# Kernel tuning notes

Hardware: AMD Instinct MI355X
Metric: run time of the kernel (lower is better)

The kernel has to match this reference:

```python
import jax, jax.numpy as jnp
import numpy as np
from jax import lax

B, L, D = 4, 4096, 1024
H = 4
DK = D // H   # head_k_dim = 256
DV = D // H   # head_v_dim = 256
HID = max(8, D // 2)  # gate trunk hidden = 512
CHUNK = 32
CONV_K = 4
EPS = 1e-5


def silu(x):
    return x * jax.nn.sigmoid(x)


def l2norm(x):
    return x * lax.rsqrt(jnp.sum(x * x, -1, keepdims=True) + 1e-6)


def causal_dwconv_silu(x, w):
    # x: (b,l,d), w: (d,k). Depthwise causal conv1d followed by SiLU (ShortConvolution).
    k = w.shape[-1]
    xp = jnp.pad(x, ((0, 0), (k - 1, 0), (0, 0))).transpose(0, 2, 1)  # (b,d,l+k-1)
    y = lax.conv_general_dilated(xp, w[:, None, :], (1,), 'VALID',
                                 feature_group_count=w.shape[0])
    return silu(y.transpose(0, 2, 1))


def delta_rule_chunkwise(q, k, v, beta, chunk=CHUNK):
    # q,k: (b,h,l,dk), v: (b,h,l,dv), beta: (b,h,l). l assumed multiple of chunk.
    b, h, l, dk = q.shape
    dv = v.shape[-1]
    n = l // chunk
    q = l2norm(q)
    k = l2norm(k)
    v = v * beta[..., None]
    kb = k * beta[..., None]
    qc = q.reshape(b, h, n, chunk, dk)
    kc = k.reshape(b, h, n, chunk, dk)
    vc = v.reshape(b, h, n, chunk, dv)
    kbc = kb.reshape(b, h, n, chunk, dk)
    # In-chunk triangular inverse: the torch loop computes (I + tril(kb k^T, -1))^{-1}
    Lm = jnp.tril(kbc @ jnp.swapaxes(kc, -1, -2), -1)  # strictly lower
    eye = jnp.eye(chunk, dtype=q.dtype)
    Tinv = jax.scipy.linalg.solve_triangular(eye + Lm, jnp.broadcast_to(eye, Lm.shape), lower=True)
    u = Tinv @ vc   # (b,h,n,c,dv)
    w = Tinv @ kbc  # (b,h,n,c,dk)
    strict = jnp.triu(jnp.ones((chunk, chunk), bool), 1)

    def step(S, inp):
        q_i, k_i, u_i, w_i = inp  # (b,h,c,d)
        attn = jnp.where(strict, 0.0, q_i @ jnp.swapaxes(k_i, -1, -2))
        u_hat = u_i - w_i @ S
        o_i = q_i @ S + attn @ u_hat
        return S + jnp.swapaxes(k_i, -1, -2) @ u_hat, o_i

    S0 = jnp.zeros((b, h, dk, dv), q.dtype)
    xs = tuple(jnp.moveaxis(t, 2, 0) for t in (qc, kc, u, w))
    S, o = lax.scan(step, S0, xs)
    o = jnp.moveaxis(o, 0, 2).reshape(b, h, l, dv)
    return o, S


def ema_rule(v, gamma):
    # v: (b,h,l,d), gamma: (b,h,l). Causal EMA: s_t = g_t*s_{t-1} + (1-g_t)*v_t
    def step(state, inp):
        v_t, g_t = inp
        state = g_t[..., None] * state + (1.0 - g_t[..., None]) * v_t
        return state, state

    s0 = jnp.zeros((v.shape[0], v.shape[1], v.shape[3]), v.dtype)
    _, out = lax.scan(step, s0, (jnp.moveaxis(v, 2, 0), jnp.moveaxis(gamma, 2, 0)))
    return jnp.moveaxis(out, 0, 2)


def hierarchical_gate(x, Wtrunk, btrunk, Wcoarse, bcoarse, Wlocal, blocal, Wglobal, bglobal, log_temp_c, log_temp_f):
    b, l, _ = x.shape
    z = silu(x @ Wtrunk.T + btrunk)  # (b,l,HID)
    tc = (jax.nn.softplus(log_temp_c) + 1e-4)[None, None, :, None]  # (1,1,h,1)
    tf = (jax.nn.softplus(log_temp_f) + 1e-4)[None, None, :, None]
    pg = jax.nn.softmax((z @ Wcoarse.T + bcoarse).reshape(b, l, H, 2) / tc, axis=-1)
    q = jax.nn.softmax((z @ Wlocal.T + blocal).reshape(b, l, H, 2) / tf, axis=-1)
    r = jax.nn.softmax((z @ Wglobal.T + bglobal).reshape(b, l, H, 2) / tf, axis=-1)
    w_v = pg[..., 0:1] * q[..., 0:1]
    w_es = pg[..., 0:1] * q[..., 1:2]
    w_d = pg[..., 1:2] * r[..., 0:1]
    w_el = pg[..., 1:2] * r[..., 1:2]
    return jnp.concatenate([w_v, w_es, w_d, w_el], axis=-1)  # (b,l,h,4)


def setup_inputs() -> dict:
    key = jax.random.key(0)
    ks = jax.random.split(key, 20)
    s = 0.02
    inp = {
        'hidden_states': jax.random.normal(ks[0], (B, L, D), jnp.float32),
        'Wq': jax.random.normal(ks[1], (D, D), jnp.float32) * s,
        'Wk': jax.random.normal(ks[2], (D, D), jnp.float32) * s,
        'Wv': jax.random.normal(ks[3], (D, D), jnp.float32) * s,
        'conv_q_w': jax.random.normal(ks[4], (D, CONV_K), jnp.float32) * 0.5,
        'conv_k_w': jax.random.normal(ks[5], (D, CONV_K), jnp.float32) * 0.5,
        'conv_v_w': jax.random.normal(ks[6], (D, CONV_K), jnp.float32) * 0.5,
        'Wb': jax.random.normal(ks[7], (H, D), jnp.float32) * s,
        'Wds': jax.random.normal(ks[8], (H, D), jnp.float32) * s,
        'bds': jnp.full((H,), -2.9444, jnp.float32),
        'Wdl': jax.random.normal(ks[9], (H, D), jnp.float32) * s,
        'bdl': jnp.full((H,), 2.9444, jnp.float32),
        'Wtrunk': jax.random.normal(ks[10], (HID, D), jnp.float32) * s,
        'btrunk': jnp.zeros((HID,), jnp.float32),
        'Wcoarse': jax.random.normal(ks[11], (H * 2, HID), jnp.float32) * s,
        'bcoarse': jnp.ones((H * 2,), jnp.float32),
        'Wlocal': jax.random.normal(ks[12], (H * 2, HID), jnp.float32) * s,
        'blocal': jnp.zeros((H * 2,), jnp.float32).at[::2].set(1.0),
        'Wglobal': jax.random.normal(ks[13], (H * 2, HID), jnp.float32) * s,
        'bglobal': jnp.zeros((H * 2,), jnp.float32).at[::2].set(1.0),
        'log_temp_c': jnp.zeros((H,), jnp.float32),  # log(1.0)
        'log_temp_f': jnp.zeros((H,), jnp.float32),
        'o_norm_w': jnp.ones((DV,), jnp.float32),
        'Wo': jax.random.normal(ks[14], (D, D), jnp.float32) * s,
    }
    return inp


def reference(hidden_states, Wq, Wk, Wv, conv_q_w, conv_k_w, conv_v_w, Wb, Wds, bds, Wdl, bdl,
              Wtrunk, btrunk, Wcoarse, bcoarse, Wlocal, blocal, Wglobal, bglobal,
              log_temp_c, log_temp_f, o_norm_w, Wo):
    x = hidden_states
    b, l, _ = x.shape
    # projections + short causal depthwise conv + SiLU
    q = causal_dwconv_silu(x @ Wq.T, conv_q_w).reshape(b, l, H, DK).transpose(0, 2, 1, 3)
    k = causal_dwconv_silu(x @ Wk.T, conv_k_w).reshape(b, l, H, DK).transpose(0, 2, 1, 3)
    v = causal_dwconv_silu(x @ Wv.T, conv_v_w).reshape(b, l, H, DV).transpose(0, 2, 1, 3)
    beta = jax.nn.sigmoid(x @ Wb.T).transpose(0, 2, 1)  # (b,h,l)
    delta_o, _ = delta_rule_chunkwise(q, k, v, beta)
    g_s = jax.nn.sigmoid(x @ Wds.T + bds).transpose(0, 2, 1)  # (b,h,l) short decay
    g_l = jax.nn.sigmoid(x @ Wdl.T + bdl).transpose(0, 2, 1)  # long decay
    ema_s = ema_rule(v, g_s)
    ema_l = ema_rule(v, g_l)
    weights = hierarchical_gate(x, Wtrunk, btrunk, Wcoarse, bcoarse, Wlocal, blocal,
                                Wglobal, bglobal, log_temp_c, log_temp_f)  # (b,l,h,4) [V,Es,D,El]
    v_b = v.transpose(0, 2, 1, 3)
    o = (weights[..., 0:1] * v_b
         + weights[..., 1:2] * ema_s.transpose(0, 2, 1, 3)
         + weights[..., 2:3] * delta_o.transpose(0, 2, 1, 3)
         + weights[..., 3:4] * ema_l.transpose(0, 2, 1, 3))
    # per-head RMSNorm
    o = o * lax.rsqrt(jnp.mean(o * o, -1, keepdims=True) + EPS) * o_norm_w
    return o.reshape(b, l, D) @ Wo.T
```

## Files before the change

kernel.cpp:

```cpp
#include <hip/hip_runtime.h>
#include <math.h>

#define BB 4
#define LL 4096
#define DD 1024
#define HH 4
#define DKk 256
#define DVv 256
#define HIDD 512
#define NC 128
#define NSEG 64
#define SEG 64

typedef unsigned short ushort_t;
typedef __attribute__((ext_vector_type(8))) short short8;
typedef __attribute__((ext_vector_type(4))) float floatx4;

__device__ __forceinline__ float sigm(float x) { return 1.f / (1.f + __expf(-x)); }

__device__ __forceinline__ float bf2f(ushort_t u) {
  union { unsigned int i; float f; } c; c.i = ((unsigned int)u) << 16; return c.f;
}
__device__ __forceinline__ ushort_t f2bf(float f) {
  union { float f; unsigned int i; } c; c.f = f;
  unsigned int lsb = (c.i >> 16) & 1u;
  return (ushort_t)((c.i + 0x7fffu + lsb) >> 16);
}
__device__ __forceinline__ void unpack2(unsigned int u, float& a, float& b) {
  union { unsigned int i; float f; } c0, c1;
  c0.i = u << 16; c1.i = u & 0xffff0000u; a = c0.f; b = c1.f;
}
__device__ __forceinline__ unsigned int pack2(float a, float b) {
  return (unsigned int)f2bf(a) | ((unsigned int)f2bf(b) << 16);
}
__device__ __forceinline__ void unpack8(const uint4 v, float* o) {
  unpack2(v.x, o[0], o[1]); unpack2(v.y, o[2], o[3]);
  unpack2(v.z, o[4], o[5]); unpack2(v.w, o[6], o[7]);
}
__device__ __forceinline__ float ubits(unsigned u) {
  union { unsigned i; float f; } c; c.i = u; return c.f;
}
__device__ __forceinline__ void split2t(float a, float b, unsigned& hi, unsigned& lo) {
  union { float f; unsigned u; } ca, cb; ca.f = a; cb.f = b;
  const unsigned ha = ca.u & 0xffff0000u, hb = cb.u & 0xffff0000u;
  hi = (ha >> 16) | hb;
  union { float f; unsigned u; } la, lb;
  la.f = a - ubits(ha); lb.f = b - ubits(hb);
  lo = (la.u >> 16) | (lb.u & 0xffff0000u);
}
__device__ __forceinline__ void gload16(const ushort_t* g, ushort_t* l) {
  __builtin_amdgcn_global_load_lds(
      (const __attribute__((address_space(1))) void*)g,
      (__attribute__((address_space(3))) void*)l, 16, 0, 0);
}

__global__ __launch_bounds__(256) void cvt_bf16_kernel(const float* __restrict__ in,
    ushort_t* __restrict__ outp, int n8)
{
  const int i = blockIdx.x * 256 + threadIdx.x;
  if (i >= n8) return;
  const float4 a = ((const float4*)in)[2*i];
  const float4 b = ((const float4*)in)[2*i + 1];
  uint4 p;
  p.x = pack2(a.x, a.y); p.y = pack2(a.z, a.w);
  p.z = pack2(b.x, b.y); p.w = pack2(b.z, b.w);
  ((uint4*)outp)[i] = p;
}

template<int ACT, int BF16OUT>
__global__ __launch_bounds__(256) void gemm_bf16(const ushort_t* __restrict__ A,
    const ushort_t* __restrict__ W, const float* __restrict__ bias,
    void* __restrict__ Cv, int M, int N, int K)
{
  __shared__ ushort_t As[128*32];
  __shared__ ushort_t Ws[128*32];
  const int tid = threadIdx.x;
  const int bm = blockIdx.y * 128, bn = blockIdx.x * 128;
  const int lane = tid & 63, wave = tid >> 6;
  const int wm = (wave >> 1) * 64, wn = (wave & 1) * 64;
  const int fr = lane & 15, fq = lane >> 4;
  const int srow = wave * 16 + (lane >> 2);
  const int scol = (lane & 3) * 8;
  const ushort_t* Ap = A + (size_t)(bm + srow) * K + scol;
  const ushort_t* Wp = W + (size_t)(bn + srow) * K + scol;
  ushort_t* AsD = &As[wave * 512];
  ushort_t* WsD = &Ws[wave * 512];
  floatx4 acc[4][4];
#pragma unroll
  for (int i = 0; i < 4; ++i)
#pragma unroll
    for (int j = 0; j < 4; ++j) acc[i][j] = (floatx4){0.f, 0.f, 0.f, 0.f};

  for (int k0 = 0; k0 < K; k0 += 32) {
    __syncthreads();
    gload16(Ap + k0, AsD);
    gload16(Ap + (size_t)64 * K + k0, AsD + 64*32);
    gload16(Wp + k0, WsD);
    gload16(Wp + (size_t)64 * K + k0, WsD + 64*32);
    __syncthreads();
    short8 af[4], bf_[4];
#pragma unroll
    for (int mt = 0; mt < 4; ++mt)
      af[mt] = *(const short8*)&As[(wm + mt*16 + fr)*32 + fq*8];
#pragma unroll
    for (int nt = 0; nt < 4; ++nt)
      bf_[nt] = *(const short8*)&Ws[(wn + nt*16 + fr)*32 + fq*8];
#pragma unroll
    for (int mt = 0; mt < 4; ++mt)
#pragma unroll
      for (int nt = 0; nt < 4; ++nt)
        acc[mt][nt] = __builtin_amdgcn_mfma_f32_16x16x32_bf16(af[mt], bf_[nt], acc[mt][nt], 0, 0, 0);
  }
#pragma unroll
  for (int mt = 0; mt < 4; ++mt) {
#pragma unroll
    for (int reg = 0; reg < 4; ++reg) {
      const int row = bm + wm + mt*16 + fq*4 + reg;
#pragma unroll
      for (int nt = 0; nt < 4; ++nt) {
        const int col = bn + wn + nt*16 + fr;
        float v = acc[mt][nt][reg];
        if (ACT == 1) { v += bias[col]; v = v * sigm(v); }
        if (BF16OUT) ((ushort_t*)Cv)[(size_t)row * N + col] = f2bf(v);
        else         ((float*)Cv)[(size_t)row * N + col] = v;
      }
    }
  }
}

__global__ __launch_bounds__(256) void conv_silu_kernel(const ushort_t* __restrict__ xin,
    const float* __restrict__ wc, ushort_t* __restrict__ outp)
{
  const size_t i8 = (size_t)blockIdx.x * 256 + threadIdx.x;
  const int d8 = (int)((i8 & 127) << 3);
  const int l  = (int)((i8 >> 7) & (LL - 1));
  const int b  = (int)(i8 >> 19);
  const ushort_t* xp = xin + i8 * 8;
  const uint4 z4 = (uint4){0u,0u,0u,0u};
  const uint4 v0 = *(const uint4*)xp;
  const uint4 v1 = (l >= 1) ? *(const uint4*)(xp - DD)   : z4;
  const uint4 v2 = (l >= 2) ? *(const uint4*)(xp - 2*DD) : z4;
  const uint4 v3 = (l >= 3) ? *(const uint4*)(xp - 3*DD) : z4;
  float x0[8], x1[8], x2[8], x3[8];
  unpack8(v0, x0); unpack8(v1, x1); unpack8(v2, x2); unpack8(v3, x3);
  unsigned pk[4];
#pragma unroll
  for (int p = 0; p < 4; ++p) {
    float o2[2];
#pragma unroll
    for (int q = 0; q < 2; ++q) {
      const int j = p*2 + q;
      const float4 w = *(const float4*)(wc + (d8 + j) * 4);
      float acc = w.w * x0[j];
      acc = fmaf(w.z, x1[j], acc);
      acc = fmaf(w.y, x2[j], acc);
      acc = fmaf(w.x, x3[j], acc);
      o2[q] = acc * sigm(acc);
    }
    pk[p] = pack2(o2[0], o2[1]);
  }
  const int h = d8 >> 8, dk = d8 & 255;
  *(uint4*)(outp + (((size_t)(b*HH + h))*LL + l)*DKk + dk) = *(uint4*)pk;
}

__global__ __launch_bounds__(256) void small_proj_kernel(const float* __restrict__ x,
   const float* __restrict__ Wb, const float* __restrict__ Wds, const float* __restrict__ bds,
   const float* __restrict__ Wdl, const float* __restrict__ bdl,
   float* __restrict__ beta, float* __restrict__ gs, float* __restrict__ gl)
{
  const int bl = blockIdx.x;
  const int t = threadIdx.x, wave = t >> 6, lane = t & 63;
  __shared__ float res[12];
  const float* xr = x + (size_t)bl * DD + lane * 16;
  const float4 x0 = *(const float4*)(xr);
  const float4 x1 = *(const float4*)(xr + 4);
  const float4 x2 = *(const float4*)(xr + 8);
  const float4 x3 = *(const float4*)(xr + 12);
  for (int rr = 0; rr < 3; ++rr) {
    const int r = wave * 3 + rr;
    const int mat = r >> 2, h = r & 3;
    const float* Wr = (mat == 0 ? Wb : (mat == 1 ? Wds : Wdl)) + (size_t)h * DD + lane * 16;
    const float4 w0 = *(const float4*)(Wr);
    const float4 w1 = *(const float4*)(Wr + 4);
    const float4 w2 = *(const float4*)(Wr + 8);
    const float4 w3 = *(const float4*)(Wr + 12);
    float p = x0.x*w0.x + x0.y*w0.y + x0.z*w0.z + x0.w*w0.w
            + x1.x*w1.x + x1.y*w1.y + x1.z*w1.z + x1.w*w1.w
            + x2.x*w2.x + x2.y*w2.y + x2.z*w2.z + x2.w*w2.w
            + x3.x*w3.x + x3.y*w3.y + x3.z*w3.z + x3.w*w3.w;
#pragma unroll
    for (int o = 1; o < 64; o <<= 1) p += __shfl_xor(p, o);
    if (lane == 0) res[r] = p;
  }
  __syncthreads();
  if (t < 12) {
    const int mat = t >> 2, h = t & 3;
    float v = res[t];
    if (mat == 1) v += bds[h];
    if (mat == 2) v += bdl[h];
    v = sigm(v);
    const int b = bl >> 12, l = bl & (LL - 1);
    const size_t o = ((size_t)(b*HH + h))*LL + l;
    (mat == 0 ? beta : (mat == 1 ? gs : gl))[o] = v;
  }
}

__global__ __launch_bounds__(256) void gate_kernel(const ushort_t* __restrict__ z,
  const float* __restrict__ Wc, const float* __restrict__ bc,
  const float* __restrict__ Wl, const float* __restrict__ bl_,
  const float* __restrict__ Wg, const float* __restrict__ bg,
  const float* __restrict__ ltc, const float* __restrict__ ltf,
  float* __restrict__ wgt)
{
  const int bl = blockIdx.x;
  const int t = threadIdx.x, wave = t >> 6, lane = t & 63;
  __shared__ float res[24];
  const uint4 zv = *(const uint4*)(z + (size_t)bl * HIDD + lane * 8);
  float zf[8]; unpack8(zv, zf);
  for (int rr = 0; rr < 6; ++rr) {
    const int r = wave * 6 + rr;
    const int mat = r >> 3, qi = r & 7;
    const float* Wr = (mat == 0 ? Wc : (mat == 1 ? Wl : Wg)) + (size_t)qi * HIDD + lane * 8;
    const float4 w0 = *(const float4*)(Wr);
    const float4 w1 = *(const float4*)(Wr + 4);
    float p = zf[0]*w0.x + zf[1]*w0.y + zf[2]*w0.z + zf[3]*w0.w
            + zf[4]*w1.x + zf[5]*w1.y + zf[6]*w1.z + zf[7]*w1.w;
#pragma unroll
    for (int o = 1; o < 64; o <<= 1) p += __shfl_xor(p, o);
    if (lane == 0) {
      const float* br = (mat == 0 ? bc : (mat == 1 ? bl_ : bg));
      res[r] = p + br[qi];
    }
  }
  __syncthreads();
  if (t < 4) {
    const float tc = logf(1.f + __expf(ltc[t])) + 1e-4f;
    const float tf = logf(1.f + __expf(ltf[t])) + 1e-4f;
    const float pg0 = sigm((res[2*t]     - res[2*t+1])     / tc);
    const float q0  = sigm((res[8+2*t]   - res[8+2*t+1])   / tf);
    const float r0  = sigm((res[16+2*t]  - res[16+2*t+1])  / tf);
    float* o = wgt + ((size_t)bl * HH + t) * 4;
    o[0] = pg0 * q0;         o[1] = pg0 * (1.f - q0);
    o[2] = (1.f - pg0) * r0; o[3] = (1.f - pg0) * (1.f - r0);
  }
}

#define QS 264
__global__ __launch_bounds__(256) void prep_kernel(ushort_t* __restrict__ q,
    ushort_t* __restrict__ k, const ushort_t* __restrict__ v,
    const float* __restrict__ beta,
    ushort_t* __restrict__ u, ushort_t* __restrict__ w,
    ushort_t* __restrict__ ah, ushort_t* __restrict__ al)
{
  __shared__ ushort_t qb[32*QS];
  __shared__ ushort_t kb[32*QS];
  __shared__ float Lm[32*32];
  __shared__ float betas[32];
  const int bid = blockIdx.x;
  const int ci = bid & (NC - 1);
  const int bh = bid >> 7;
  const int t = threadIdx.x;
  const size_t base = ((size_t)bh * LL + ci*32) * DKk;
  if (t < 32) betas[t] = beta[(size_t)bh * LL + ci*32 + t];
  for (int i4 = t; i4 < 1024; i4 += 256) {
    const int r = i4 >> 5, e = (i4 & 31) * 8;
    *(uint4*)&qb[r*QS + e] = *(const uint4*)(q + base + r*256 + e);
    *(uint4*)&kb[r*QS + e] = *(const uint4*)(k + base + r*256 + e);
  }
  __syncthreads();
  {
    const int r = t >> 3, g = t & 7;
    float sq = 0.f, sk = 0.f;
    for (int e = g*32; e < g*32 + 32; ++e) {
      const float a = bf2f(qb[r*QS + e]); sq = fmaf(a, a, sq);
      const float c = bf2f(kb[r*QS + e]); sk = fmaf(c, c, sk);
    }
#pragma unroll
    for (int o = 1; o < 8; o <<= 1) { sq += __shfl_xor(sq, o); sk += __shfl_xor(sk, o); }
    const float rq = rsqrtf(sq + 1e-6f), rk = rsqrtf(sk + 1e-6f);
    for (int e = g*32; e < g*32 + 32; ++e) {
      qb[r*QS + e] = f2bf(bf2f(qb[r*QS + e]) * rq);
      kb[r*QS + e] = f2bf(bf2f(kb[r*QS + e]) * rk);
    }
  }
  __syncthreads();
  for (int i4 = t; i4 < 1024; i4 += 256) {
    const int r = i4 >> 5, e = (i4 & 31) * 8;
    *(uint4*)(q + base + r*256 + e) = *(const uint4*)&qb[r*QS + e];
  }
  {
    unsigned int pk[16];
#pragma unroll
    for (int j = 0; j < 16; ++j)
      pk[j] = (unsigned int)kb[(2*j)*QS + t] | ((unsigned int)kb[(2*j+1)*QS + t] << 16);
    uint4* kd = (uint4*)(k + base + (size_t)t*32);
#pragma unroll
    for (int j = 0; j < 4; ++j) kd[j] = ((const uint4*)pk)[j];
  }
  {
    const int lane = t & 63, wv4 = t >> 6;
    const int fr = lane & 15, fq = lane >> 4;
    const int it = wv4 >> 1, jt = wv4 & 1;
    floatx4 dq = (floatx4){0.f,0.f,0.f,0.f};
    floatx4 dk2 = (floatx4){0.f,0.f,0.f,0.f};
#pragma unroll
    for (int ks = 0; ks < 8; ++ks) {
      const short8 bfk = *(const short8*)&kb[(jt*16+fr)*QS + ks*32 + fq*8];
      const short8 afq = *(const short8*)&qb[(it*16+fr)*QS + ks*32 + fq*8];
      const short8 afk = *(const short8*)&kb[(it*16+fr)*QS + ks*32 + fq*8];
      dq  = __builtin_amdgcn_mfma_f32_16x16x32_bf16(afq, bfk, dq, 0,0,0);
      dk2 = __builtin_amdgcn_mfma_f32_16x16x32_bf16(afk, bfk, dk2, 0,0,0);
    }
#pragma unroll
    for (int reg = 0; reg < 4; ++reg) {
      const int i = it*16 + fq*4 + reg;
      const int j = jt*16 + fr;
      const float av = (j <= i) ? dq[reg] : 0.f;
      const ushort_t hh = f2bf(av);
      const size_t aoff = ((size_t)bh*NC + ci)*1024 + (size_t)i*32 + j;
      ah[aoff] = hh;
      al[aoff] = f2bf(av - bf2f(hh));
      Lm[i*32 + j] = (j < i) ? betas[i] * dk2[reg] : 0.f;
    }
  }
  __syncthreads();
  {
    float cu[32], cw[32];
#pragma unroll
    for (int r = 0; r < 32; ++r) {
      cu[r] = bf2f(v[base + r*256 + t]) * betas[r];
      cw[r] = bf2f(kb[r*QS + t]) * betas[r];
    }
#pragma unroll
    for (int i = 1; i < 32; ++i) {
      float au = cu[i], aw = cw[i];
#pragma unroll
      for (int j = 0; j < i; ++j) {
        const float lm = Lm[i*32 + j];
        au = fmaf(-lm, cu[j], au);
        aw = fmaf(-lm, cw[j], aw);
      }
      cu[i] = au; cw[i] = aw;
    }
    {
      unsigned int pu[16];
#pragma unroll
      for (int j = 0; j < 16; ++j) pu[j] = pack2(cu[2*j], cu[2*j+1]);
      uint4* ud = (uint4*)(u + base + (size_t)t*32);
#pragma unroll
      for (int j = 0; j < 4; ++j) ud[j] = ((const uint4*)pu)[j];
    }
#pragma unroll
    for (int r = 0; r < 32; ++r) w[base + r*256 + t] = f2bf(cw[r]);
  }
}

#define S16(dv,kk) (((dv)<<8) + ((kk) ^ (((dv)&7)<<3)))
#define U16(dv,cr) (((dv)<<5) + ((cr) ^ (((dv)&3)<<3)))

__global__ __launch_bounds__(256, 2) void scan_kernel(
    const ushort_t* __restrict__ qn, const ushort_t* __restrict__ kt,
    const ushort_t* __restrict__ ut, const ushort_t* __restrict__ w,
    const ushort_t* __restrict__ ah, const ushort_t* __restrict__ al,
    float* __restrict__ dout)
{
  __shared__ ushort_t STh[16*256];
  __shared__ ushort_t STl[16*256];
  __shared__ ushort_t Uh[16*32];
  __shared__ ushort_t Ul[16*32];
  const int bid = blockIdx.x;
  const int bh = bid & 15, vs = bid >> 4;
  const int b = bh >> 2, h = bh & 3;
  const int t = threadIdx.x, lane = t & 63, wv = t >> 6;
  const int fr = lane & 15, fq = lane >> 4;
  const int mt = wv & 1;
  const bool isW = (wv < 2);

  for (int i = t; i < 512; i += 256) {
    ((uint4*)STh)[i] = (uint4){0u,0u,0u,0u};
    ((uint4*)STl)[i] = (uint4){0u,0u,0u,0u};
  }

  const size_t bhL = (size_t)bh * LL;
  const ushort_t* wqB = (isW ? w : qn) + bhL * DKk;
  const ushort_t* kB  = kt + bhL * DKk;
  const ushort_t* uB  = ut + bhL * DVv;
  const ushort_t* ahB = ah + (size_t)bh * NC * 1024;
  const ushort_t* alB = al + (size_t)bh * NC * 1024;
  float* oB = dout + (size_t)b * LL * DD + h * DVv + vs * 8 + fr;

  floatx4 Sacc[4];
#pragma unroll
  for (int i = 0; i < 4; ++i) Sacc[i] = (floatx4){0.f,0.f,0.f,0.f};

  short8 aw[8]; uint2 uu;
  auto loadA = [&](int ci) {
    const ushort_t* ap = wqB + (size_t)(ci*32 + mt*16 + fr) * DKk + fq*8;
#pragma unroll
    for (int ks = 0; ks < 8; ++ks) aw[ks] = *(const short8*)(ap + ks*32);
    if (isW)
      uu = *(const uint2*)(uB + (size_t)ci*8192 + (size_t)(vs*8 + (fr & 7))*32 + mt*16 + fq*4);
  };

  loadA(0);
  __syncthreads();

  for (int ci = 0; ci < NC; ++ci) {
    short8 kf[4];
    {
      const ushort_t* kp = kB + (size_t)ci*8192 + (size_t)(wv*64 + fr)*32 + fq*8;
#pragma unroll
      for (int m = 0; m < 4; ++m) kf[m] = *(const short8*)(kp + m*512);
    }
    short8 afh, afl;
    if (!isW) {
      afh = *(const short8*)(ahB + (size_t)ci*1024 + (mt*16+fr)*32 + fq*8);
      afl = *(const short8*)(alB + (size_t)ci*1024 + (mt*16+fr)*32 + fq*8);
    }
    floatx4 acc0, acc1;
    if (isW) {
      float u0,u1,u2,u3; unpack2(uu.x,u0,u1); unpack2(uu.y,u2,u3);
      acc0 = (floatx4){-u0,-u1,-u2,-u3};
      acc1 = (floatx4){0.f,0.f,0.f,0.f};
#pragma unroll
      for (int ks = 0; ks < 8; ++ks) {
        const short8 sh = *(const short8*)&STh[S16(fr, ks*32 + fq*8)];
        const short8 sl = *(const short8*)&STl[S16(fr, ks*32 + fq*8)];
        acc0 = __builtin_amdgcn_mfma_f32_16x16x32_bf16(aw[ks], sh, acc0, 0,0,0);
        acc1 = __builtin_amdgcn_mfma_f32_16x16x32_bf16(aw[ks], sl, acc1, 0,0,0);
      }
      const float v0 = -(acc0[0]+acc1[0]), v1 = -(acc0[1]+acc1[1]);
      const float v2 = -(acc0[2]+acc1[2]), v3 = -(acc0[3]+acc1[3]);
      unsigned ph0, pl0, ph1, pl1;
      split2t(v0, v1, ph0, pl0); split2t(v2, v3, ph1, pl1);
      *(uint2*)&Uh[U16(fr, mt*16 + fq*4)] = (uint2){ph0, ph1};
      *(uint2*)&Ul[U16(fr, mt*16 + fq*4)] = (uint2){pl0, pl1};
    } else {
      acc0 = (floatx4){0.f,0.f,0.f,0.f};
#pragma unroll
      for (int ks = 0; ks < 8; ++ks) {
        const short8 sh = *(const short8*)&STh[S16(fr, ks*32 + fq*8)];
        acc0 = __builtin_amdgcn_mfma_f32_16x16x32_bf16(aw[ks], sh, acc0, 0,0,0);
      }
    }
    __syncthreads();
    if (ci + 1 < NC) loadA(ci + 1);
    const short8 uhh = *(const short8*)&Uh[U16(fr, fq*8)];
    const short8 uhl = *(const short8*)&Ul[U16(fr, fq*8)];
    if (!isW) {
      acc0 = __builtin_amdgcn_mfma_f32_16x16x32_bf16(afh, uhh, acc0, 0,0,0);
      acc0 = __builtin_amdgcn_mfma_f32_16x16x32_bf16(afh, uhl, acc0, 0,0,0);
      acc0 = __builtin_amdgcn_mfma_f32_16x16x32_bf16(afl, uhh, acc0, 0,0,0);
      if (fr < 8) {
        float* op = oB + (size_t)(ci*32 + mt*16 + fq*4) * DD;
#pragma unroll
        for (int r = 0; r < 4; ++r) op[(size_t)r * DD] = acc0[r];
      }
    }
#pragma unroll
    for (int m = 0; m < 4; ++m) {
      Sacc[m] = __builtin_amdgcn_mfma_f32_16x16x32_bf16(kf[m], uhh, Sacc[m], 0,0,0);
      Sacc[m] = __builtin_amdgcn_mfma_f32_16x16x32_bf16(kf[m], uhl, Sacc[m], 0,0,0);
    }
#pragma unroll
    for (int m = 0; m < 4; ++m) {
      unsigned ph0, pl0, ph1, pl1;
      split2t(Sacc[m][0], Sacc[m][1], ph0, pl0);
      split2t(Sacc[m][2], Sacc[m][3], ph1, pl1);
      const int dk0 = wv*64 + m*16 + fq*4;
      *(uint2*)&STh[S16(fr, dk0)] = (uint2){ph0, ph1};
      *(uint2*)&STl[S16(fr, dk0)] = (uint2){pl0, pl1};
    }
    __syncthreads();
  }
}

__global__ __launch_bounds__(256) void ema_local_kernel(const ushort_t* __restrict__ v,
  const float* __restrict__ gs, const float* __restrict__ gl,
  ushort_t* __restrict__ es, ushort_t* __restrict__ el,
  float* __restrict__ Bs, float* __restrict__ Bl,
  float* __restrict__ As, float* __restrict__ Al,
  float* __restrict__ PfS, float* __restrict__ PfL)
{
  const int bid = blockIdx.x;
  const int seg = bid & (NSEG - 1), bh = bid >> 6;
  const int b = bh >> 2, h = bh & 3;
  const int dv = threadIdx.x;
  const int l0 = seg * SEG;
  const ushort_t* vp = v + ((size_t)bh*LL + l0) * DVv + dv;
  const float* gsp = gs + (size_t)bh*LL + l0;
  const float* glp = gl + (size_t)bh*LL + l0;
  ushort_t* esp = es + ((size_t)b*LL + l0)*DD + h*DVv + dv;
  ushort_t* elp = el + ((size_t)b*LL + l0)*DD + h*DVv + dv;
  float* pfs = PfS + (size_t)bh*LL + l0;
  float* pfl = PfL + (size_t)bh*LL + l0;
  float s1 = 0.f, s2 = 0.f, p1 = 1.f, p2 = 1.f;
  for (int j = 0; j < SEG; ++j) {
    const float vv = bf2f(vp[(size_t)j * DVv]);
    const float a = gsp[j], g2 = glp[j];
    s1 = fmaf(a,  s1, (1.f - a)  * vv);
    s2 = fmaf(g2, s2, (1.f - g2) * vv);
    p1 *= a; p2 *= g2;
    esp[(size_t)j * DD] = f2bf(s1);
    elp[(size_t)j * DD] = f2bf(s2);
    if (dv == 0) { pfs[j] = p1; pfl[j] = p2; }
  }
  const size_t o = (((size_t)bh*NSEG + seg) << 8) + dv;
  Bs[o] = s1; Bl[o] = s2;
  if (dv == 0) { As[bh*NSEG + seg] = p1; Al[bh*NSEG + seg] = p2; }
}

__global__ __launch_bounds__(256) void ema_carry_kernel(
  const float* __restrict__ Bs, const float* __restrict__ Bl,
  const float* __restrict__ As, const float* __restrict__ Al,
  float* __restrict__ Cs, float* __restrict__ Cl)
{
  const int bh = blockIdx.x;
  const int dv = threadIdx.x;
  __shared__ float Ash[NSEG], Alh[NSEG];
  if (dv < NSEG) { Ash[dv] = As[bh*NSEG + dv]; Alh[dv] = Al[bh*NSEG + dv]; }
  __syncthreads();
  float c1 = 0.f, c2 = 0.f;
  for (int s = 0; s < NSEG; ++s) {
    const size_t o = (((size_t)bh*NSEG + s) << 8) + dv;
    Cs[o] = c1; Cl[o] = c2;
    c1 = fmaf(Ash[s], c1, Bs[o]);
    c2 = fmaf(Alh[s], c2, Bl[o]);
  }
}

__global__ __launch_bounds__(64) void combine_kernel(const ushort_t* __restrict__ v,
  const ushort_t* __restrict__ es, const ushort_t* __restrict__ el,
  const float* __restrict__ dov, const float* __restrict__ wgt,
  const float* __restrict__ onw,
  const float* __restrict__ Cs, const float* __restrict__ Cl,
  const float* __restrict__ PfS, const float* __restrict__ PfL,
  ushort_t* __restrict__ outp)
{
  const int bid = blockIdx.x;
  const int h = bid & 3;
  const size_t bl = (size_t)(bid >> 2);
  const int lane = threadIdx.x;
  const size_t b = bl >> 12;
  const size_t l = bl & (LL - 1);
  const int bh = (int)(b * HH) + h;
  const int seg = (int)(l >> 6);
  const size_t vidx = (((b*HH + h) * (size_t)LL) + l) * DVv + lane*4;
  const size_t didx = bl * DD + h*DVv + lane*4;
  const uint2 vu = *(const uint2*)(v + vidx);
  const uint2 eu = *(const uint2*)(es + didx);
  const uint2 gu = *(const uint2*)(el + didx);
  const float4 d4 = *(const float4*)(dov + didx);
  const float pS = PfS[(size_t)bh*LL + l];
  const float pL = PfL[(size_t)bh*LL + l];
  const float4 cs4 = *(const float4*)(Cs + (((size_t)bh*NSEG + seg) << 8) + lane*4);
  const float4 cl4 = *(const float4*)(Cl + (((size_t)bh*NSEG + seg) << 8) + lane*4);
  float vf[4], ef[4], gf[4];
  unpack2(vu.x, vf[0], vf[1]); unpack2(vu.y, vf[2], vf[3]);
  unpack2(eu.x, ef[0], ef[1]); unpack2(eu.y, ef[2], ef[3]);
  unpack2(gu.x, gf[0], gf[1]); unpack2(gu.y, gf[2], gf[3]);
  ef[0] = fmaf(pS, cs4.x, ef[0]); ef[1] = fmaf(pS, cs4.y, ef[1]);
  ef[2] = fmaf(pS, cs4.z, ef[2]); ef[3] = fmaf(pS, cs4.w, ef[3]);
  gf[0] = fmaf(pL, cl4.x, gf[0]); gf[1] = fmaf(pL, cl4.y, gf[1]);
  gf[2] = fmaf(pL, cl4.z, gf[2]); gf[3] = fmaf(pL, cl4.w, gf[3]);
  const float* wp = wgt + (size_t)bid * 4;
  const float w0 = wp[0], w1 = wp[1], w2 = wp[2], w3 = wp[3];
  float o[4];
  const float df[4] = {d4.x, d4.y, d4.z, d4.w};
  float ss = 0.f;
#pragma unroll
  for (int i = 0; i < 4; ++i) {
    o[i] = w0*vf[i] + w1*ef[i] + w2*df[i] + w3*gf[i];
    ss = fmaf(o[i], o[i], ss);
  }
#pragma unroll
  for (int off = 1; off < 64; off <<= 1) ss += __shfl_xor(ss, off);
  const float sc = rsqrtf(ss * (1.f / DVv) + 1e-5f);
  const float4 nw = *(const float4*)(onw + lane*4);
  uint2 pk;
  pk.x = pack2(o[0]*sc*nw.x, o[1]*sc*nw.y);
  pk.y = pack2(o[2]*sc*nw.z, o[3]*sc*nw.w);
  *(uint2*)(outp + didx) = pk;
}

extern "C" void kernel_launch(void* const* d_in, const int* in_sizes, int n_in,
                              void* d_out, int out_size, void* d_ws, size_t ws_size,
                              hipStream_t stream)
{
  const float* x    = (const float*)d_in[0];
  const float* Wq   = (const float*)d_in[1];
  const float* Wk   = (const float*)d_in[2];
  const float* Wv   = (const float*)d_in[3];
  const float* cqw  = (const float*)d_in[4];
  const float* ckw  = (const float*)d_in[5];
  const float* cvw  = (const float*)d_in[6];
  const float* Wb   = (const float*)d_in[7];
  const float* Wds  = (const float*)d_in[8];
  const float* bds  = (const float*)d_in[9];
  const float* Wdl  = (const float*)d_in[10];
  const float* bdl  = (const float*)d_in[11];
  const float* Wtr  = (const float*)d_in[12];
  const float* btr  = (const float*)d_in[13];
  const float* Wc   = (const float*)d_in[14];
  const float* bc   = (const float*)d_in[15];
  const float* Wl   = (const float*)d_in[16];
  const float* blc  = (const float*)d_in[17];
  const float* Wg   = (const float*)d_in[18];
  const float* bg   = (const float*)d_in[19];
  const float* ltc  = (const float*)d_in[20];
  const float* ltf  = (const float*)d_in[21];
  const float* onw  = (const float*)d_in[22];
  const float* Wo   = (const float*)d_in[23];
  float* outp = (float*)d_out;

  const size_t BLD = (size_t)BB * LL * DD;
  unsigned char* w8 = (unsigned char*)d_ws;
  const size_t SL = BLD * 2;
  ushort_t* SA = (ushort_t*)(w8 + 0*SL);
  ushort_t* SB = (ushort_t*)(w8 + 1*SL);
  ushort_t* SC = (ushort_t*)(w8 + 2*SL);
  ushort_t* SD = (ushort_t*)(w8 + 3*SL);
  ushort_t* SE = (ushort_t*)(w8 + 4*SL);
  ushort_t* zb   = (ushort_t*)(w8 + 5*SL);
  ushort_t* attn_hi = (ushort_t*)(w8 + 5*SL + BLD);
  ushort_t* attn_lo = attn_hi + (size_t)BB*HH*NC*1024;
  float*    beta = (float*)(attn_hi + 2*(size_t)BB*HH*NC*1024);
  float*    gs   = beta + (size_t)BB*HH*LL;
  float*    gl   = gs   + (size_t)BB*HH*LL;
  float*    wgt  = gl   + (size_t)BB*HH*LL;
  float*    Bs   = wgt  + (size_t)BB*LL*HH*4;
  float*    Bl   = Bs   + (size_t)BB*HH*NSEG*256;
  float*    Cs   = Bl   + (size_t)BB*HH*NSEG*256;
  float*    Cl   = Cs   + (size_t)BB*HH*NSEG*256;
  float*    As   = Cl   + (size_t)BB*HH*NSEG*256;
  float*    Al   = As   + (size_t)BB*HH*NSEG;
  float*    PfS  = Al   + (size_t)BB*HH*NSEG;
  float*    PfL  = PfS  + (size_t)BB*HH*LL;
  ushort_t* Wqb  = (ushort_t*)(PfL + (size_t)BB*HH*LL);
  ushort_t* Wkb  = Wqb + (size_t)DD*DD;
  ushort_t* Wvb  = Wkb + (size_t)DD*DD;
  ushort_t* Wob  = Wvb + (size_t)DD*DD;
  ushort_t* Wtrb = Wob + (size_t)DD*DD;
  ushort_t* xb   = SD;
  float*    dov  = outp;

  const int MBL = BB * LL;
  dim3 blk256(256);

  cvt_bf16_kernel<<<dim3((unsigned)(BLD/8/256)), blk256, 0, stream>>>(x, xb, (int)(BLD/8));
  cvt_bf16_kernel<<<dim3(DD*DD/8/256), blk256, 0, stream>>>(Wq, Wqb, DD*DD/8);
  cvt_bf16_kernel<<<dim3(DD*DD/8/256), blk256, 0, stream>>>(Wk, Wkb, DD*DD/8);
  cvt_bf16_kernel<<<dim3(DD*DD/8/256), blk256, 0, stream>>>(Wv, Wvb, DD*DD/8);
  cvt_bf16_kernel<<<dim3(DD*DD/8/256), blk256, 0, stream>>>(Wo, Wob, DD*DD/8);
  cvt_bf16_kernel<<<dim3(HIDD*DD/8/256), blk256, 0, stream>>>(Wtr, Wtrb, HIDD*DD/8);

  gemm_bf16<0,1><<<dim3(DD/128, MBL/128), blk256, 0, stream>>>(xb, Wqb, nullptr, SA, MBL, DD, DD);
  gemm_bf16<0,1><<<dim3(DD/128, MBL/128), blk256, 0, stream>>>(xb, Wkb, nullptr, SB, MBL, DD, DD);
  gemm_bf16<0,1><<<dim3(DD/128, MBL/128), blk256, 0, stream>>>(xb, Wvb, nullptr, SC, MBL, DD, DD);
  gemm_bf16<1,1><<<dim3(HIDD/128, MBL/128), blk256, 0, stream>>>(xb, Wtrb, btr, zb, MBL, HIDD, DD);
  small_proj_kernel<<<dim3(MBL), blk256, 0, stream>>>(x, Wb, Wds, bds, Wdl, bdl, beta, gs, gl);
  gate_kernel<<<dim3(MBL), blk256, 0, stream>>>(zb, Wc, bc, Wl, blc, Wg, bg, ltc, ltf, wgt);
  conv_silu_kernel<<<dim3((unsigned)(BLD/8/256)), blk256, 0, stream>>>(SA, cqw, SD);
  conv_silu_kernel<<<dim3((unsigned)(BLD/8/256)), blk256, 0, stream>>>(SB, ckw, SA);
  conv_silu_kernel<<<dim3((unsigned)(BLD/8/256)), blk256, 0, stream>>>(SC, cvw, SB);
  prep_kernel<<<dim3(BB*HH*NC), blk256, 0, stream>>>(SD, SA, SB, beta, SC, SE, attn_hi, attn_lo);
  scan_kernel<<<dim3(512), blk256, 0, stream>>>(SD, SA, SC, SE, attn_hi, attn_lo, dov);
  ema_local_kernel<<<dim3(BB*HH*NSEG), blk256, 0, stream>>>(SB, gs, gl, SE, SD, Bs, Bl, As, Al, PfS, PfL);
  ema_carry_kernel<<<dim3(BB*HH), blk256, 0, stream>>>(Bs, Bl, As, Al, Cs, Cl);
  combine_kernel<<<dim3(MBL*HH), dim3(64), 0, stream>>>(SB, SE, SD, dov, wgt, onw, Cs, Cl, PfS, PfL, SA);
  gemm_bf16<0,0><<<dim3(DD/128, MBL/128), blk256, 0, stream>>>(SA, Wob, nullptr, outp, MBL, DD, DD);
}
```

Before: 1.145 ms.

## Merge bf16 conversions, fold gate into scan launch, widen scan value slices

All six fp32-to-bf16 conversions now run in one kernel launch instead of six. The gate projection moves into extra blocks of the scan kernel, so those blocks can fill idle CUs while the 256 scan blocks run their long sequential loop. The scan now gives each block 16 value columns instead of 8, which halves its block count, and its launch bound changes from 2 blocks per CU to 1. The l2norm in the prep kernel also switches to vectorized register-held loads and stores. The risk is that fewer scan blocks expose less parallelism for the sequential scan. A block's scheduling order may also leave gate blocks contending with scan blocks.

```diff
diff --git a/kernel.cpp b/kernel.cpp
--- a/kernel.cpp
+++ b/kernel.cpp
@@ -54,17 +54,38 @@
       (__attribute__((address_space(3))) void*)l, 16, 0, 0);
 }
 
-__global__ __launch_bounds__(256) void cvt_bf16_kernel(const float* __restrict__ in,
-    ushort_t* __restrict__ outp, int n8)
-{
-  const int i = blockIdx.x * 256 + threadIdx.x;
-  if (i >= n8) return;
-  const float4 a = ((const float4*)in)[2*i];
-  const float4 b = ((const float4*)in)[2*i + 1];
+__global__ __launch_bounds__(256) void cvt_all_kernel(
+    const float* __restrict__ x,  const float* __restrict__ Wq,
+    const float* __restrict__ Wk, const float* __restrict__ Wv,
+    const float* __restrict__ Wo, const float* __restrict__ Wtr,
+    ushort_t* __restrict__ xb,  ushort_t* __restrict__ Wqb,
+    ushort_t* __restrict__ Wkb, ushort_t* __restrict__ Wvb,
+    ushort_t* __restrict__ Wob, ushort_t* __restrict__ Wtrb)
+{
+  const int NX = (int)((size_t)BB*LL*DD/8), NW = DD*DD/8, NT = HIDD*DD/8;
+  int i = blockIdx.x * 256 + threadIdx.x;
+  const float* src; ushort_t* dst;
+  if (i < NX) { src = x; dst = xb; }
+  else {
+    i -= NX;
+    if (i < NW) { src = Wq; dst = Wqb; }
+    else { i -= NW;
+      if (i < NW) { src = Wk; dst = Wkb; }
+      else { i -= NW;
+        if (i < NW) { src = Wv; dst = Wvb; }
+        else { i -= NW;
+          if (i < NW) { src = Wo; dst = Wob; }
+          else { i -= NW; if (i >= NT) return; src = Wtr; dst = Wtrb; }
+        }
+      }
+    }
+  }
+  const float4 a = ((const float4*)src)[2*i];
+  const float4 b = ((const float4*)src)[2*i + 1];
   uint4 p;
   p.x = pack2(a.x, a.y); p.y = pack2(a.z, a.w);
   p.z = pack2(b.x, b.y); p.w = pack2(b.z, b.w);
-  ((uint4*)outp)[i] = p;
+  ((uint4*)dst)[i] = p;
 }
 
 template<int ACT, int BF16OUT>
@@ -205,46 +226,6 @@
   }
 }
 
-__global__ __launch_bounds__(256) void gate_kernel(const ushort_t* __restrict__ z,
-  const float* __restrict__ Wc, const float* __restrict__ bc,
-  const float* __restrict__ Wl, const float* __restrict__ bl_,
-  const float* __restrict__ Wg, const float* __restrict__ bg,
-  const float* __restrict__ ltc, const float* __restrict__ ltf,
-  float* __restrict__ wgt)
-{
-  const int bl = blockIdx.x;
-  const int t = threadIdx.x, wave = t >> 6, lane = t & 63;
-  __shared__ float res[24];
-  const uint4 zv = *(const uint4*)(z + (size_t)bl * HIDD + lane * 8);
-  float zf[8]; unpack8(zv, zf);
-  for (int rr = 0; rr < 6; ++rr) {
-    const int r = wave * 6 + rr;
-    const int mat = r >> 3, qi = r & 7;
-    const float* Wr = (mat == 0 ? Wc : (mat == 1 ? Wl : Wg)) + (size_t)qi * HIDD + lane * 8;
-    const float4 w0 = *(const float4*)(Wr);
-    const float4 w1 = *(const float4*)(Wr + 4);
-    float p = zf[0]*w0.x + zf[1]*w0.y + zf[2]*w0.z + zf[3]*w0.w
-            + zf[4]*w1.x + zf[5]*w1.y + zf[6]*w1.z + zf[7]*w1.w;
-#pragma unroll
-    for (int o = 1; o < 64; o <<= 1) p += __shfl_xor(p, o);
-    if (lane == 0) {
-      const float* br = (mat == 0 ? bc : (mat == 1 ? bl_ : bg));
-      res[r] = p + br[qi];
-    }
-  }
-  __syncthreads();
-  if (t < 4) {
-    const float tc = logf(1.f + __expf(ltc[t])) + 1e-4f;
-    const float tf = logf(1.f + __expf(ltf[t])) + 1e-4f;
-    const float pg0 = sigm((res[2*t]     - res[2*t+1])     / tc);
-    const float q0  = sigm((res[8+2*t]   - res[8+2*t+1])   / tf);
-    const float r0  = sigm((res[16+2*t]  - res[16+2*t+1])  / tf);
-    float* o = wgt + ((size_t)bl * HH + t) * 4;
-    o[0] = pg0 * q0;         o[1] = pg0 * (1.f - q0);
-    o[2] = (1.f - pg0) * r0; o[3] = (1.f - pg0) * (1.f - r0);
-  }
-}
-
 #define QS 264
 __global__ __launch_bounds__(256) void prep_kernel(ushort_t* __restrict__ q,
     ushort_t* __restrict__ k, const ushort_t* __restrict__ v,
@@ -270,17 +251,36 @@
   __syncthreads();
   {
     const int r = t >> 3, g = t & 7;
+    const int e0 = g * 32;
+    float qf[32], kf[32];
+#pragma unroll
+    for (int j = 0; j < 4; ++j) {
+      const uint4 qv = *(const uint4*)&qb[r*QS + e0 + j*8];
+      const uint4 kv = *(const uint4*)&kb[r*QS + e0 + j*8];
+      unpack8(qv, qf + j*8); unpack8(kv, kf + j*8);
+    }
     float sq = 0.f, sk = 0.f;
-    for (int e = g*32; e < g*32 + 32; ++e) {
-      const float a = bf2f(qb[r*QS + e]); sq = fmaf(a, a, sq);
-      const float c = bf2f(kb[r*QS + e]); sk = fmaf(c, c, sk);
+#pragma unroll
+    for (int j = 0; j < 32; ++j) {
+      sq = fmaf(qf[j], qf[j], sq);
+      sk = fmaf(kf[j], kf[j], sk);
     }
 #pragma unroll
     for (int o = 1; o < 8; o <<= 1) { sq += __shfl_xor(sq, o); sk += __shfl_xor(sk, o); }
     const float rq = rsqrtf(sq + 1e-6f), rk = rsqrtf(sk + 1e-6f);
-    for (int e = g*32; e < g*32 + 32; ++e) {
-      qb[r*QS + e] = f2bf(bf2f(qb[r*QS + e]) * rq);
-      kb[r*QS + e] = f2bf(bf2f(kb[r*QS + e]) * rk);
+#pragma unroll
+    for (int j = 0; j < 4; ++j) {
+      uint4 qo, ko;
+      qo.x = pack2(qf[j*8+0]*rq, qf[j*8+1]*rq);
+      qo.y = pack2(qf[j*8+2]*rq, qf[j*8+3]*rq);
+      qo.z = pack2(qf[j*8+4]*rq, qf[j*8+5]*rq);
+      qo.w = pack2(qf[j*8+6]*rq, qf[j*8+7]*rq);
+      ko.x = pack2(kf[j*8+0]*rk, kf[j*8+1]*rk);
+      ko.y = pack2(kf[j*8+2]*rk, kf[j*8+3]*rk);
+      ko.z = pack2(kf[j*8+4]*rk, kf[j*8+5]*rk);
+      ko.w = pack2(kf[j*8+6]*rk, kf[j*8+7]*rk);
+      *(uint4*)&qb[r*QS + e0 + j*8] = qo;
+      *(uint4*)&kb[r*QS + e0 + j*8] = ko;
     }
   }
   __syncthreads();
@@ -358,20 +358,63 @@
 #define S16(dv,kk) (((dv)<<8) + ((kk) ^ (((dv)&7)<<3)))
 #define U16(dv,cr) (((dv)<<5) + ((cr) ^ (((dv)&3)<<3)))
 
-__global__ __launch_bounds__(256, 2) void scan_kernel(
+__global__ __launch_bounds__(256, 1) void scan_gate_kernel(
     const ushort_t* __restrict__ qn, const ushort_t* __restrict__ kt,
     const ushort_t* __restrict__ ut, const ushort_t* __restrict__ w,
     const ushort_t* __restrict__ ah, const ushort_t* __restrict__ al,
-    float* __restrict__ dout)
+    float* __restrict__ dout,
+    const ushort_t* __restrict__ z,
+    const float* __restrict__ Wc, const float* __restrict__ bc,
+    const float* __restrict__ Wl, const float* __restrict__ bl_,
+    const float* __restrict__ Wg, const float* __restrict__ bg,
+    const float* __restrict__ ltc, const float* __restrict__ ltf,
+    float* __restrict__ wgt)
 {
   __shared__ ushort_t STh[16*256];
   __shared__ ushort_t STl[16*256];
   __shared__ ushort_t Uh[16*32];
   __shared__ ushort_t Ul[16*32];
   const int bid = blockIdx.x;
+  const int t = threadIdx.x;
+
+  if (bid >= 256) {
+    const int bl = bid - 256;
+    const int wave = t >> 6, lane = t & 63;
+    float* res = (float*)STh;
+    const uint4 zv = *(const uint4*)(z + (size_t)bl * HIDD + lane * 8);
+    float zf[8]; unpack8(zv, zf);
+    for (int rr = 0; rr < 6; ++rr) {
+      const int r = wave * 6 + rr;
+      const int mat = r >> 3, qi = r & 7;
+      const float* Wr = (mat == 0 ? Wc : (mat == 1 ? Wl : Wg)) + (size_t)qi * HIDD + lane * 8;
+      const float4 w0 = *(const float4*)(Wr);
+      const float4 w1 = *(const float4*)(Wr + 4);
+      float p = zf[0]*w0.x + zf[1]*w0.y + zf[2]*w0.z + zf[3]*w0.w
+              + zf[4]*w1.x + zf[5]*w1.y + zf[6]*w1.z + zf[7]*w1.w;
+#pragma unroll
+      for (int o = 1; o < 64; o <<= 1) p += __shfl_xor(p, o);
+      if (lane == 0) {
+        const float* br = (mat == 0 ? bc : (mat == 1 ? bl_ : bg));
+        res[r] = p + br[qi];
+      }
+    }
+    __syncthreads();
+    if (t < 4) {
+      const float tc = logf(1.f + __expf(ltc[t])) + 1e-4f;
+      const float tf = logf(1.f + __expf(ltf[t])) + 1e-4f;
+      const float pg0 = sigm((res[2*t]     - res[2*t+1])     / tc);
+      const float q0  = sigm((res[8+2*t]   - res[8+2*t+1])   / tf);
+      const float r0  = sigm((res[16+2*t]  - res[16+2*t+1])  / tf);
+      float* o = wgt + ((size_t)bl * HH + t) * 4;
+      o[0] = pg0 * q0;         o[1] = pg0 * (1.f - q0);
+      o[2] = (1.f - pg0) * r0; o[3] = (1.f - pg0) * (1.f - r0);
+    }
+    return;
+  }
+
   const int bh = bid & 15, vs = bid >> 4;
   const int b = bh >> 2, h = bh & 3;
-  const int t = threadIdx.x, lane = t & 63, wv = t >> 6;
+  const int lane = t & 63, wv = t >> 6;
   const int fr = lane & 15, fq = lane >> 4;
   const int mt = wv & 1;
   const bool isW = (wv < 2);
@@ -387,7 +430,7 @@
   const ushort_t* uB  = ut + bhL * DVv;
   const ushort_t* ahB = ah + (size_t)bh * NC * 1024;
   const ushort_t* alB = al + (size_t)bh * NC * 1024;
-  float* oB = dout + (size_t)b * LL * DD + h * DVv + vs * 8 + fr;
+  float* oB = dout + (size_t)b * LL * DD + h * DVv + vs * 16 + fr;
 
   floatx4 Sacc[4];
 #pragma unroll
@@ -399,7 +442,7 @@
 #pragma unroll
     for (int ks = 0; ks < 8; ++ks) aw[ks] = *(const short8*)(ap + ks*32);
     if (isW)
-      uu = *(const uint2*)(uB + (size_t)ci*8192 + (size_t)(vs*8 + (fr & 7))*32 + mt*16 + fq*4);
+      uu = *(const uint2*)(uB + (size_t)ci*8192 + (size_t)(vs*16 + fr)*32 + mt*16 + fq*4);
   };
 
   loadA(0);
@@ -451,11 +494,9 @@
       acc0 = __builtin_amdgcn_mfma_f32_16x16x32_bf16(afh, uhh, acc0, 0,0,0);
       acc0 = __builtin_amdgcn_mfma_f32_16x16x32_bf16(afh, uhl, acc0, 0,0,0);
       acc0 = __builtin_amdgcn_mfma_f32_16x16x32_bf16(afl, uhh, acc0, 0,0,0);
-      if (fr < 8) {
-        float* op = oB + (size_t)(ci*32 + mt*16 + fq*4) * DD;
-#pragma unroll
-        for (int r = 0; r < 4; ++r) op[(size_t)r * DD] = acc0[r];
-      }
+      float* op = oB + (size_t)(ci*32 + mt*16 + fq*4) * DD;
+#pragma unroll
+      for (int r = 0; r < 4; ++r) op[(size_t)r * DD] = acc0[r];
     }
 #pragma unroll
     for (int m = 0; m < 4; ++m) {
@@ -647,24 +688,24 @@
   const int MBL = BB * LL;
   dim3 blk256(256);
 
-  cvt_bf16_kernel<<<dim3((unsigned)(BLD/8/256)), blk256, 0, stream>>>(x, xb, (int)(BLD/8));
-  cvt_bf16_kernel<<<dim3(DD*DD/8/256), blk256, 0, stream>>>(Wq, Wqb, DD*DD/8);
-  cvt_bf16_kernel<<<dim3(DD*DD/8/256), blk256, 0, stream>>>(Wk, Wkb, DD*DD/8);
-  cvt_bf16_kernel<<<dim3(DD*DD/8/256), blk256, 0, stream>>>(Wv, Wvb, DD*DD/8);
-  cvt_bf16_kernel<<<dim3(DD*DD/8/256), blk256, 0, stream>>>(Wo, Wob, DD*DD/8);
-  cvt_bf16_kernel<<<dim3(HIDD*DD/8/256), blk256, 0, stream>>>(Wtr, Wtrb, HIDD*DD/8);
+  {
+    const int NTOT = (int)(BLD/8) + 4*(DD*DD/8) + HIDD*DD/8;
+    cvt_all_kernel<<<dim3((NTOT + 255)/256), blk256, 0, stream>>>(
+        x, Wq, Wk, Wv, Wo, Wtr, xb, Wqb, Wkb, Wvb, Wob, Wtrb);
+  }
 
   gemm_bf16<0,1><<<dim3(DD/128, MBL/128), blk256, 0, stream>>>(xb, Wqb, nullptr, SA, MBL, DD, DD);
   gemm_bf16<0,1><<<dim3(DD/128, MBL/128), blk256, 0, stream>>>(xb, Wkb, nullptr, SB, MBL, DD, DD);
   gemm_bf16<0,1><<<dim3(DD/128, MBL/128), blk256, 0, stream>>>(xb, Wvb, nullptr, SC, MBL, DD, DD);
   gemm_bf16<1,1><<<dim3(HIDD/128, MBL/128), blk256, 0, stream>>>(xb, Wtrb, btr, zb, MBL, HIDD, DD);
   small_proj_kernel<<<dim3(MBL), blk256, 0, stream>>>(x, Wb, Wds, bds, Wdl, bdl, beta, gs, gl);
-  gate_kernel<<<dim3(MBL), blk256, 0, stream>>>(zb, Wc, bc, Wl, blc, Wg, bg, ltc, ltf, wgt);
   conv_silu_kernel<<<dim3((unsigned)(BLD/8/256)), blk256, 0, stream>>>(SA, cqw, SD);
   conv_silu_kernel<<<dim3((unsigned)(BLD/8/256)), blk256, 0, stream>>>(SB, ckw, SA);
   conv_silu_kernel<<<dim3((unsigned)(BLD/8/256)), blk256, 0, stream>>>(SC, cvw, SB);
   prep_kernel<<<dim3(BB*HH*NC), blk256, 0, stream>>>(SD, SA, SB, beta, SC, SE, attn_hi, attn_lo);
-  scan_kernel<<<dim3(512), blk256, 0, stream>>>(SD, SA, SC, SE, attn_hi, attn_lo, dov);
+  scan_gate_kernel<<<dim3(256 + MBL), blk256, 0, stream>>>(
+      SD, SA, SC, SE, attn_hi, attn_lo, dov,
+      zb, Wc, bc, Wl, blc, Wg, bg, ltc, ltf, wgt);
   ema_local_kernel<<<dim3(BB*HH*NSEG), blk256, 0, stream>>>(SB, gs, gl, SE, SD, Bs, Bl, As, Al, PfS, PfL);
   ema_carry_kernel<<<dim3(BB*HH), blk256, 0, stream>>>(Bs, Bl, As, Al, Cs, Cl);
   combine_kernel<<<dim3(MBL*HH), dim3(64), 0, stream>>>(SB, SE, SD, dov, wgt, onw, Cs, Cl, PfS, PfL, SA);
```

Result: faster. 1.046 ms (-8.7%).
